# Optimization experiments

Measured on AMD Instinct MI355X. Metric: run time of the kernel, lower is better.

The kernel has to match this reference:

```python
import jax, jax.numpy as jnp
import numpy as np

WORLD_SIZE = 8
M = 4096
N = 4096
K_LOCAL = 1024  # full K = WORLD_SIZE * K_LOCAL = 8192


def setup_inputs() -> dict:
    key = jax.random.key(0)
    k1, k2 = jax.random.split(key)
    # Per-rank activation shard [R, M, K_local] and weight shard [R, N, K_local]
    inp = jax.random.normal(k1, (WORLD_SIZE, M, K_LOCAL), dtype=jnp.float32) * 0.02
    w = jax.random.normal(k2, (WORLD_SIZE, N, K_LOCAL), dtype=jnp.float32) * 0.02
    return {"input": inp, "weight": w}


def reference(input, weight):
    # Each rank r computes a partial GEMM: input[r] @ weight[r].T -> [M, N].
    # Reduce(-scatter) sums partials over ranks; the single einsum contracts
    # both the rank axis (the all-reduce part) and K_local (the GEMM part).
    full = jnp.einsum("rmk,rnk->mn", input, weight)  # [M, N]
    R = input.shape[0]
    # Scatter: rank r receives rows [r*M/R : (r+1)*M/R] -> stacked [R, M/R, N]
    return full.reshape(R, full.shape[0] // R, full.shape[1])
```

## Files before the change

kernel.cpp:

```cpp
#include <hip/hip_runtime.h>
#include <cstdint>
#include <cstddef>


#define M_DIM 4096
#define N_DIM 4096
#define K_DIM 8192
#define K_LOCAL 1024
#define RANKS 8

typedef __bf16 bf16x8 __attribute__((ext_vector_type(8)));
typedef float f32x4 __attribute__((ext_vector_type(4)));

__device__ __forceinline__ unsigned short f2bf(float f) {
    unsigned int u = __float_as_uint(f);
    unsigned int r = (u + 0x7fffu + ((u >> 16) & 1u)) >> 16;
    return (unsigned short)r;
}

__global__ __launch_bounds__(256) void convert_cast(
    const float* __restrict__ srcA, unsigned short* __restrict__ dstA,
    const float* __restrict__ srcB, unsigned short* __restrict__ dstB,
    int blocks_per_tensor) {
    const float* src = srcA;
    unsigned short* dst = dstA;
    int b = blockIdx.x;
    if (b >= blocks_per_tensor) { b -= blocks_per_tensor; src = srcB; dst = dstB; }
    size_t base = (size_t)b * 4096 + threadIdx.x * 4;
#pragma unroll
    for (int i = 0; i < 4; ++i) {
        size_t e = base + i * 1024;
        f32x4 v = __builtin_nontemporal_load((const f32x4*)(src + e));
        ushort4 o;
        o.x = f2bf(v.x); o.y = f2bf(v.y); o.z = f2bf(v.z); o.w = f2bf(v.w);
        *(ushort4*)(dst + e) = o;
    }
}

__device__ __forceinline__ void gll16(const unsigned short* g, unsigned short* l) {
    __builtin_amdgcn_global_load_lds(
        (const __attribute__((address_space(1))) void*)g,
        (__attribute__((address_space(3))) void*)l,
        16, 0, 0);
}

__device__ __forceinline__ int k_off(int t) {
    return ((t >> 4) << 22) | ((t & 15) << 6);
}

#define VM0 asm volatile("s_waitcnt vmcnt(0)" ::: "memory")
#define VMNONE ((void)0)
#define BAR __builtin_amdgcn_s_barrier();

#define STAGE_A(TOFF, HALF, PBUF) { \
    _Pragma("unroll") for (int j_ = 0; j_ < 2; ++j_) \
        gll16(A + (size_t)((TOFF) + (HALF) * 131072 + thrA[j_]), \
              smem + (PBUF) * 16384 + (HALF) * 8192 + ldsOff[j_]); }

#define STAGE_B(TOFF, HALF, PBUF) { \
    _Pragma("unroll") for (int j_ = 0; j_ < 2; ++j_) \
        gll16(B + (size_t)((TOFF) + (HALF) * 131072 + thrB[j_]), \
              smem + 32768 + (PBUF) * 16384 + (HALF) * 8192 + ldsOff[j_]); }

#define READ_A(DST, BASE, MOFF) { \
    _Pragma("unroll") for (int ks_ = 0; ks_ < 2; ++ks_) \
        _Pragma("unroll") for (int mm_ = 0; mm_ < 4; ++mm_) \
            DST[ks_][mm_] = *(const bf16x8*)&(BASE)[(((MOFF) + mm_) * 16 + l15) * 64 + (ks_ ? swz1 : swz0)]; }

#define READ_B(DST, BASE, NJ0) { \
    _Pragma("unroll") for (int ks_ = 0; ks_ < 2; ++ks_) \
        _Pragma("unroll") for (int nn_ = 0; nn_ < 2; ++nn_) \
            DST[ks_][nn_] = *(const bf16x8*)&(BASE)[(bRowBase + ((NJ0) + nn_) * 16 + l15) * 64 + (ks_ ? swz1 : swz0)]; }

#define QUAD(AF, BF, MI0, NJ0) { \
    __builtin_amdgcn_s_setprio(1); \
    _Pragma("unroll") for (int ks_ = 0; ks_ < 2; ++ks_) \
        _Pragma("unroll") for (int mm_ = 0; mm_ < 4; ++mm_) \
            _Pragma("unroll") for (int nn_ = 0; nn_ < 2; ++nn_) \
                acc[(MI0) + mm_][(NJ0) + nn_] = __builtin_amdgcn_mfma_f32_16x16x32_bf16( \
                    AF[ks_][mm_], BF[ks_][nn_], acc[(MI0) + mm_][(NJ0) + nn_], 0, 0, 0); \
    __builtin_amdgcn_s_setprio(0); }

#define KTILE(PBUF, KT, S, SR, VMOP) { \
    const int t1off_ = k_off((KT) + 1); \
    unsigned short* aC_ = smem + (PBUF) * 16384 + wmIdx * 8192; \
    unsigned short* bC_ = smem + 32768 + (PBUF) * 16384 + bHalfSel * 8192; \
    unsigned short* aN_ = smem + ((PBUF) ^ 1) * 16384 + wmIdx * 8192; \
    unsigned short* bN_ = smem + 32768 + ((PBUF) ^ 1) * 16384 + bHalfSel * 8192; \
     \
    READ_A(aHi, aC_, 4) \
    if (S) { STAGE_A(t1off_, 0, (PBUF) ^ 1) STAGE_A(t1off_, 1, (PBUF) ^ 1) \
             STAGE_B(t1off_, 0, (PBUF) ^ 1) STAGE_B(t1off_, 1, (PBUF) ^ 1) } \
    QUAD(aLo, bLo, 0, 0) \
    READ_B(bHi, bC_, 2) \
    QUAD(aHi, bLo, 4, 0) \
    QUAD(aLo, bHi, 0, 2) \
    VMOP; \
    BAR \
    __builtin_amdgcn_sched_barrier(0); \
     \
    if (SR) { READ_A(aLo, aN_, 0) READ_B(bLo, bN_, 0) } \
    QUAD(aHi, bHi, 4, 2) \
}

__global__ __launch_bounds__(512, 2) void gemm_bf16_8ph(
    const unsigned short* __restrict__ A,
    const unsigned short* __restrict__ B,
    float* __restrict__ C) {
    extern __shared__ unsigned short smem[];

    const int tid = threadIdx.x;
    const int lane = tid & 63;
    const int wave = tid >> 6;
    const int wmIdx = wave >> 2;
    const int wn = wave & 3;
    const int l15 = lane & 15;
    const int l4 = lane >> 4;
    const int bHalfSel = wn >> 1;
    const int bRowBase = (wn & 1) * 64;

    const int bid = blockIdx.x;
    const int xcd = bid & 7;
    const int idx = bid >> 3;
    const int tm = (xcd >> 2) * 8 + (idx >> 2);
    const int tn = (xcd & 3) * 4 + (idx & 3);
    const int bm0 = tm * 256;
    const int bn0 = tn * 256;

    int thrA[2], thrB[2], ldsOff[2];
#pragma unroll
    for (int j = 0; j < 2; ++j) {
        int cc = j * 512 + tid;
        int row = cc >> 3;
        int col = ((cc & 7) ^ (row & 7)) * 8;
        thrA[j] = (bm0 + row) * K_LOCAL + col;
        thrB[j] = (bn0 + row) * K_LOCAL + col;
        ldsOff[j] = cc * 8;
    }

    const int swz0 = ((0 + l4) ^ (l15 & 7)) * 8;
    const int swz1 = ((4 + l4) ^ (l15 & 7)) * 8;

    bf16x8 aLo[2][4], aHi[2][4], bLo[2][2], bHi[2][2];
    f32x4 acc[8][4] = {};

    STAGE_A(0, 0, 0)
    STAGE_A(0, 1, 0)
    STAGE_B(0, 0, 0)
    STAGE_B(0, 1, 0)
    VM0;
    BAR
    READ_A(aLo, smem + wmIdx * 8192, 0)
    READ_B(bLo, smem + 32768 + bHalfSel * 8192, 0)

#pragma unroll 1
    for (int kt = 0; kt < 126; kt += 2) {
        KTILE(0, kt, 1, 1, VM0)
        KTILE(1, kt + 1, 1, 1, VM0)
    }
    KTILE(0, 126, 1, 1, VM0)
    KTILE(1, 127, 0, 0, VMNONE)

#pragma unroll
    for (int mi = 0; mi < 8; ++mi) {
        int row0 = bm0 + wmIdx * 128 + mi * 16 + l4 * 4;
#pragma unroll
        for (int nj = 0; nj < 4; ++nj) {
            int col = bn0 + wn * 64 + nj * 16 + l15;
#pragma unroll
            for (int r = 0; r < 4; ++r)
                C[(size_t)(row0 + r) * N_DIM + col] = acc[mi][nj][r];
        }
    }
}

__global__ __launch_bounds__(256) void gemm_bf16_128(
    const unsigned short* __restrict__ A,
    const unsigned short* __restrict__ B,
    float* __restrict__ C) {
    __shared__ __align__(16) unsigned short As[128 * 64];
    __shared__ __align__(16) unsigned short Bs[128 * 64];

    const int tid = threadIdx.x;
    const int lane = tid & 63;
    const int wave = tid >> 6;
    const int wm = (wave >> 1) * 64;
    const int wnn = (wave & 1) * 64;
    const int l15 = lane & 15;
    const int l4 = lane >> 4;

    const int bid = blockIdx.x;
    const int xcd = bid & 7;
    const int q = bid >> 3;
    const int st = (q >> 2) * 8 + xcd;
    const int pos = q & 3;
    const int bm0 = ((st >> 4) * 2 + (pos >> 1)) * 128;
    const int bn0 = ((st & 15) * 2 + (pos & 1)) * 128;

    const unsigned short* ga[4];
    const unsigned short* gb[4];
    int lo[4];
#pragma unroll
    for (int p = 0; p < 4; ++p) {
        int cc = p * 256 + tid;
        int row = cc >> 3;
        int cpos = cc & 7;
        int col = (cpos ^ (row & 7)) * 8;
        ga[p] = A + (size_t)(bm0 + row) * K_LOCAL + col;
        gb[p] = B + (size_t)(bn0 + row) * K_LOCAL + col;
        lo[p] = cc * 8;
    }

    const int swz0 = ((l4 + 0) ^ (l15 & 7)) * 8;
    const int swz1 = ((l4 + 4) ^ (l15 & 7)) * 8;
    const int a_row = (wm + l15) * 64;
    const int b_row = (wnn + l15) * 64;

    f32x4 acc[4][4] = {};

    for (int r = 0; r < RANKS; ++r) {
        const size_t roff = (size_t)r * (M_DIM * (size_t)K_LOCAL);
        for (int kl = 0; kl < K_LOCAL; kl += 64) {
#pragma unroll
            for (int p = 0; p < 4; ++p) {
                gll16(ga[p] + roff + kl, &As[lo[p]]);
                gll16(gb[p] + roff + kl, &Bs[lo[p]]);
            }
            __syncthreads();
#pragma unroll
            for (int ks = 0; ks < 2; ++ks) {
                const int swz = ks ? swz1 : swz0;
                bf16x8 af[4], bfr[4];
#pragma unroll
                for (int i = 0; i < 4; ++i)
                    af[i] = *(const bf16x8*)&As[a_row + i * 16 * 64 + swz];
#pragma unroll
                for (int j = 0; j < 4; ++j)
                    bfr[j] = *(const bf16x8*)&Bs[b_row + j * 16 * 64 + swz];
#pragma unroll
                for (int i = 0; i < 4; ++i)
#pragma unroll
                    for (int j = 0; j < 4; ++j)
                        acc[i][j] = __builtin_amdgcn_mfma_f32_16x16x32_bf16(
                            af[i], bfr[j], acc[i][j], 0, 0, 0);
            }
            __syncthreads();
        }
    }

#pragma unroll
    for (int i = 0; i < 4; ++i) {
        int row0 = bm0 + wm + i * 16 + l4 * 4;
#pragma unroll
        for (int j = 0; j < 4; ++j) {
            int col = bn0 + wnn + j * 16 + l15;
#pragma unroll
            for (int r = 0; r < 4; ++r)
                C[(size_t)(row0 + r) * N_DIM + col] = acc[i][j][r];
        }
    }
}

__global__ void gemm_naive(const float* __restrict__ A, const float* __restrict__ B,
                           float* __restrict__ C) {
    __shared__ float As[16][17];
    __shared__ float Bs[16][17];
    int tx = threadIdx.x, ty = threadIdx.y;
    int m = blockIdx.y * 16 + ty;
    int n0 = blockIdx.x * 16;
    float accv = 0.f;
    for (int kt = 0; kt < K_DIM; kt += 16) {
        int r = kt >> 10;
        int k = (kt & 1023) + tx;
        As[ty][tx] = A[((size_t)r * M_DIM + m) * K_LOCAL + k];
        Bs[ty][tx] = B[((size_t)r * N_DIM + (n0 + ty)) * K_LOCAL + k];
        __syncthreads();
#pragma unroll
        for (int kk = 0; kk < 16; ++kk) accv += As[ty][kk] * Bs[tx][kk];
        __syncthreads();
    }
    C[(size_t)m * N_DIM + n0 + tx] = accv;
}

extern "C" void kernel_launch(void* const* d_in, const int* in_sizes, int n_in,
                              void* d_out, int out_size, void* d_ws, size_t ws_size,
                              hipStream_t stream) {
    const float* inp = (const float*)d_in[0];
    const float* wgt = (const float*)d_in[1];
    float* out = (float*)d_out;

    const size_t elems = (size_t)M_DIM * K_DIM;
    const size_t need = 2 * elems * sizeof(unsigned short);

    if (ws_size >= need) {
        unsigned short* Abf = (unsigned short*)d_ws;
        unsigned short* Bbf = Abf + elems;
        const int bpt = (int)(elems / 4096);
        convert_cast<<<bpt * 2, 256, 0, stream>>>(inp, Abf, wgt, Bbf, bpt);

        static int dynOK = -1;
        if (dynOK < 0) {
            dynOK = (hipFuncSetAttribute((const void*)gemm_bf16_8ph,
                                         hipFuncAttributeMaxDynamicSharedMemorySize,
                                         131072) == hipSuccess)
                        ? 1
                        : 0;
        }
        if (dynOK) {
            gemm_bf16_8ph<<<256, 512, 131072, stream>>>(Abf, Bbf, out);
        } else {
            gemm_bf16_128<<<1024, 256, 0, stream>>>(Abf, Bbf, out);
        }
    } else {
        dim3 grid(N_DIM / 16, M_DIM / 16);
        dim3 block(16, 16);
        gemm_naive<<<grid, block, 0, stream>>>(inp, wgt, out);
    }
}
```

Measured before the change: 259.3 us.

## Restructure K-loop pipeline to span tile boundaries with a two-tile-ahead prefetch

Reorganizes the main GEMM loop so each iteration finishes the second half of the current tile's MFMAs, reads the full next tile's fragments from LDS, issues global staging for the tile two steps ahead, and starts the next tile's first MFMAs before the barrier. A prologue now preloads both tile 0 and tile 1 and computes the first half-tile. The aim is to put more MFMA work between the global loads and the barrier wait, and to hide LDS read latency across the sync point. In exchange, all A/B fragments for the next tile are live at once, which raises register pressure, and the schedule is more sensitive to how the compiler orders instructions.

```diff
diff --git a/kernel.cpp b/kernel.cpp
--- a/kernel.cpp
+++ b/kernel.cpp
@@ -81,26 +81,20 @@
                     AF[ks_][mm_], BF[ks_][nn_], acc[(MI0) + mm_][(NJ0) + nn_], 0, 0, 0); \
     __builtin_amdgcn_s_setprio(0); }
 
-#define KTILE(PBUF, KT, S, SR, VMOP) { \
-    const int t1off_ = k_off((KT) + 1); \
-    unsigned short* aC_ = smem + (PBUF) * 16384 + wmIdx * 8192; \
-    unsigned short* bC_ = smem + 32768 + (PBUF) * 16384 + bHalfSel * 8192; \
-    unsigned short* aN_ = smem + ((PBUF) ^ 1) * 16384 + wmIdx * 8192; \
-    unsigned short* bN_ = smem + 32768 + ((PBUF) ^ 1) * 16384 + bHalfSel * 8192; \
-     \
-    READ_A(aHi, aC_, 4) \
-    if (S) { STAGE_A(t1off_, 0, (PBUF) ^ 1) STAGE_A(t1off_, 1, (PBUF) ^ 1) \
-             STAGE_B(t1off_, 0, (PBUF) ^ 1) STAGE_B(t1off_, 1, (PBUF) ^ 1) } \
-    QUAD(aLo, bLo, 0, 0) \
-    READ_B(bHi, bC_, 2) \
-    QUAD(aHi, bLo, 4, 0) \
-    QUAD(aLo, bHi, 0, 2) \
+#define KINT(PN, KT, S, SR, VMOP) { \
+    unsigned short* aN_ = smem + (PN) * 16384 + wmIdx * 8192; \
+    unsigned short* bN_ = smem + 32768 + (PN) * 16384 + bHalfSel * 8192; \
+    const int t2off_ = k_off((KT) + 2); \
+    QUAD(aLo, bHi, 0, 2)                               \
+    if (SR) { READ_A(aLo, aN_, 0) READ_B(bLo, bN_, 0) } \
+    QUAD(aHi, bHi, 4, 2)                               \
+    if (SR) { READ_A(aHi, aN_, 4) READ_B(bHi, bN_, 2) } \
+    if (S) { STAGE_A(t2off_, 0, (PN) ^ 1) STAGE_A(t2off_, 1, (PN) ^ 1) \
+             STAGE_B(t2off_, 0, (PN) ^ 1) STAGE_B(t2off_, 1, (PN) ^ 1) } \
+    if (SR) { QUAD(aLo, bLo, 0, 0) QUAD(aHi, bLo, 4, 0) }   \
     VMOP; \
     BAR \
     __builtin_amdgcn_sched_barrier(0); \
-     \
-    if (SR) { READ_A(aLo, aN_, 0) READ_B(bLo, bN_, 0) } \
-    QUAD(aHi, bHi, 4, 2) \
 }
 
 __global__ __launch_bounds__(512, 2) void gemm_bf16_8ph(
@@ -150,16 +144,34 @@
     STAGE_B(0, 1, 0)
     VM0;
     BAR
-    READ_A(aLo, smem + wmIdx * 8192, 0)
-    READ_B(bLo, smem + 32768 + bHalfSel * 8192, 0)
+    {
+        unsigned short* a0_ = smem + wmIdx * 8192;
+        unsigned short* b0_ = smem + 32768 + bHalfSel * 8192;
+        READ_A(aLo, a0_, 0)
+        READ_B(bLo, b0_, 0)
+        READ_A(aHi, a0_, 4)
+        READ_B(bHi, b0_, 2)
+    }
+    {
+        const int t1off = k_off(1);
+        STAGE_A(t1off, 0, 1)
+        STAGE_A(t1off, 1, 1)
+        STAGE_B(t1off, 0, 1)
+        STAGE_B(t1off, 1, 1)
+    }
+    QUAD(aLo, bLo, 0, 0)
+    QUAD(aHi, bLo, 4, 0)
+    VM0;
+    BAR
+    __builtin_amdgcn_sched_barrier(0);
 
 #pragma unroll 1
     for (int kt = 0; kt < 126; kt += 2) {
-        KTILE(0, kt, 1, 1, VM0)
-        KTILE(1, kt + 1, 1, 1, VM0)
-    }
-    KTILE(0, 126, 1, 1, VM0)
-    KTILE(1, 127, 0, 0, VMNONE)
+        KINT(1, kt, 1, 1, VM0)
+        KINT(0, kt + 1, 1, 1, VM0)
+    }
+    KINT(1, 126, 0, 1, VMNONE)
+    KINT(0, 127, 0, 0, VMNONE)
 
 #pragma unroll
     for (int mi = 0; mi < 8; ++mi) {
```

Measured after the change: 273.1 us. 1.05x slower.
